# Optimization experiments

Measured on AMD Instinct MI355X. Metric: run time of the kernel, lower is better.

Reference implementation:

```python
import jax, jax.numpy as jnp
import numpy as np

T, B, E, H, F = 1024, 2, 1024, 16, 8
D = E // H
R = 2 * T - 1  # relative positions T-1 .. -(T-1)


def setup_inputs() -> dict:
    key = jax.random.key(0)
    ks = jax.random.split(key, 11)
    std = float(np.sqrt(2.0 / (E + E)))
    return {
        "input": jax.random.normal(ks[0], (T, B, E), jnp.float32),
        "pos": jax.random.normal(ks[1], (R, B, E), jnp.float32),
        "factor": jax.random.normal(ks[2], (F,), jnp.float32),
        "in_proj_weight": jax.random.normal(ks[3], (3 * E * E, F), jnp.float32) * std,
        "pos_proj_weight": jax.random.normal(ks[4], (E * E, F), jnp.float32) * std,
        "out_proj_weight": jax.random.normal(ks[5], (E * E, F), jnp.float32) * std,
        "in_proj_bias": jax.random.normal(ks[6], (3 * E, F), jnp.float32) * 0.02,
        "pos_proj_bias": jax.random.normal(ks[7], (E, F), jnp.float32) * 0.02,
        "out_proj_bias": jax.random.normal(ks[8], (E, F), jnp.float32) * 0.02,
        "r_w_bias": jax.random.normal(ks[9], (E, F), jnp.float32) * 0.02,
        "r_r_bias": jax.random.normal(ks[10], (E, F), jnp.float32) * 0.02,
    }


def _rel_shift(x):
    # x: [BH, T, R] -> out[b, i, j] = x[b, i, j + (T-1) - i]
    bh, q, r = x.shape
    zp = jnp.zeros((bh, q, 1), x.dtype)
    xp = jnp.concatenate([zp, x], axis=2).reshape(bh, r + 1, q)
    return xp[:, 1:, :].reshape(bh, q, r)


def reference(input, pos, factor, in_proj_weight, pos_proj_weight, out_proj_weight,
              in_proj_bias, pos_proj_bias, out_proj_bias, r_w_bias, r_r_bias):
    # hypernetwork: generate effective weights from factor vector (torch.mv)
    W_in = (in_proj_weight @ factor).reshape(3 * E, E)
    W_pos = (pos_proj_weight @ factor).reshape(E, E)
    W_out = (out_proj_weight @ factor).reshape(E, E)
    b_in = in_proj_bias @ factor
    b_pos = pos_proj_bias @ factor
    b_out = out_proj_bias @ factor
    rw = (r_w_bias @ factor).reshape(H, D)  # content bias
    rr = (r_r_bias @ factor).reshape(H, D)  # position bias

    qkv = input @ W_in.T + b_in                      # [T, B, 3E]
    q, k, v = jnp.split(qkv, 3, axis=-1)
    q = q.reshape(T, B, H, D)
    k = k.reshape(T, B, H, D)
    v = v.reshape(T, B, H, D)
    r = (pos @ W_pos.T + b_pos).reshape(R, B, H, D)  # [R, B, H, D]

    scale = 1.0 / np.sqrt(D)
    # AC: content-content + content bias term
    AC = jnp.einsum('ibhd,jbhd->bhij', q + rw, k)    # [B, H, T, T]
    # BD: content-position + position bias term, then relative shift
    BD = jnp.einsum('ibhd,rbhd->bhir', q + rr, r)    # [B, H, T, R]
    BD = _rel_shift(BD.reshape(B * H, T, R))[:, :, :T].reshape(B, H, T, T)

    attn = jax.nn.softmax((AC + BD) * scale, axis=-1)  # [B, H, T, T]
    out = jnp.einsum('bhij,jbhd->ibhd', attn, v).reshape(T, B, E)
    out = out @ W_out.T + b_out                       # [T, B, E]
    return out
```

## Files before the change

kernel.cpp:

```cpp
#include <hip/hip_runtime.h>


typedef _Float16 h16;
typedef _Float16 h16x8 __attribute__((ext_vector_type(8)));
typedef _Float16 h16x4 __attribute__((ext_vector_type(4)));
typedef float f32x4 __attribute__((ext_vector_type(4)));

static __device__ __forceinline__ f32x4 mfma16(h16x8 a, h16x8 b, f32x4 c) {
  return __builtin_amdgcn_mfma_f32_16x16x32_f16(a, b, c, 0, 0, 0);
}
static __device__ __forceinline__ void gload16(const void* g, void* l) {
  __builtin_amdgcn_global_load_lds((const __attribute__((address_space(1))) void*)g,
                                   (__attribute__((address_space(3))) void*)l, 16, 0, 0);
}

__global__ __launch_bounds__(256) void hypernet_kernel(
    const float* __restrict__ fac,
    const float* __restrict__ w_in, const float* __restrict__ w_pos,
    const float* __restrict__ w_out, const float* __restrict__ b_in_w,
    const float* __restrict__ b_pos_w, const float* __restrict__ b_out_w,
    const float* __restrict__ rw_w, const float* __restrict__ rr_w,
    h16* __restrict__ Wall,
    float* __restrict__ bin, float* __restrict__ bpos, float* __restrict__ bout,
    float* __restrict__ rw, float* __restrict__ rr, h16* __restrict__ rb,
    const float* __restrict__ input, const float* __restrict__ pos,
    h16* __restrict__ cast_h)
{
  const int tid = threadIdx.x;
  const float f0=fac[0],f1=fac[1],f2=fac[2],f3=fac[3],
              f4=fac[4],f5=fac[5],f6=fac[6],f7=fac[7];
#define DOT(a,b) ((a).x*f0+(a).y*f1+(a).z*f2+(a).w*f3+(b).x*f4+(b).y*f5+(b).z*f6+(b).w*f7)

  if (blockIdx.x < 2560) {
    const int base = blockIdx.x * 2048 + tid;
    float4 va[8], vb[8];
#pragma unroll
    for (int k = 0; k < 8; ++k) {
      int r = base + k*256;
      const float4* s;
      if (r < 3145728)      s = reinterpret_cast<const float4*>(w_in  + (size_t)r*8);
      else if (r < 4194304) s = reinterpret_cast<const float4*>(w_pos + (size_t)(r-3145728)*8);
      else                  s = reinterpret_cast<const float4*>(w_out + (size_t)(r-4194304)*8);
      va[k] = s[0]; vb[k] = s[1];
    }
#pragma unroll
    for (int k = 0; k < 8; ++k)
      Wall[base + k*256] = (h16)DOT(va[k], vb[k]);
    return;
  }
  if (blockIdx.x < 2596) {
    int idx = (blockIdx.x - 2560) * 256 + tid;
    if (idx < 3072) {
      const float4* s = reinterpret_cast<const float4*>(b_in_w + (size_t)idx*8);
      bin[idx] = DOT(s[0], s[1]); return;
    }
    idx -= 3072;
    if (idx < 1024) {
      const float4* s = reinterpret_cast<const float4*>(b_pos_w + (size_t)idx*8);
      bpos[idx] = DOT(s[0], s[1]); return;
    }
    idx -= 1024;
    if (idx < 1024) {
      const float4* s = reinterpret_cast<const float4*>(b_out_w + (size_t)idx*8);
      bout[idx] = DOT(s[0], s[1]); return;
    }
    idx -= 1024;
    if (idx < 1024) {
      const float4* s = reinterpret_cast<const float4*>(rw_w + (size_t)idx*8);
      rw[idx] = DOT(s[0], s[1]); return;
    }
    idx -= 1024;
    if (idx < 1024) {
      const float4* s = reinterpret_cast<const float4*>(rr_w + (size_t)idx*8);
      rr[idx] = DOT(s[0], s[1]); return;
    }
    idx -= 1024;
    if (idx < 2048)
      rb[(((size_t)(idx >> 6)) << 17) + 2047*64 + (idx & 63)] = (h16)0.f;
    return;
  }
  {
    const int base = (blockIdx.x - 2596) * 2048 + tid;
    float4 v[8]; int g[8];
#pragma unroll
    for (int k = 0; k < 8; ++k) {
      g[k] = base + k*256;
      if (g[k] < 1572352)
        v[k] = (g[k] < 524288) ? reinterpret_cast<const float4*>(input)[g[k]]
                               : reinterpret_cast<const float4*>(pos)[g[k] - 524288];
    }
#pragma unroll
    for (int k = 0; k < 8; ++k)
      if (g[k] < 1572352) {
        h16x4 o = { (h16)v[k].x, (h16)v[k].y, (h16)v[k].z, (h16)v[k].w };
        reinterpret_cast<h16x4*>(cast_h)[g[k]] = o;
      }
  }
#undef DOT
}

template <int MODE>
__global__ __launch_bounds__(256) void gemm_lds_kernel(
    const h16* __restrict__ A, const h16* __restrict__ Bw,
    const float* __restrict__ bias, int M, int N, int K,
    float* __restrict__ Cout,
    const float* __restrict__ rwv, const float* __restrict__ rrv,
    h16* __restrict__ o0, h16* __restrict__ o1,
    h16* __restrict__ o2, h16* __restrict__ o3)
{
  __shared__ __align__(16) h16 a_sm[128*64];
  __shared__ __align__(16) h16 b_sm[128*64];
  const int tid = threadIdx.x, lane = tid & 63, wave = tid >> 6;
  const int quad = lane >> 4, t16 = lane & 15;
  const int wm = wave >> 1, wn = wave & 1;
  const int m0 = blockIdx.y * 128, n0 = blockIdx.x * 128;
  const int lrow = lane >> 3, lgran = lane & 7;
  const int gsw = (lgran ^ lrow) * 8;
  const int xg0 = (quad ^ (t16 & 7)) * 8;
  const int xg1 = xg0 ^ 32;

  f32x4 acc[4][4];
#pragma unroll
  for (int i = 0; i < 4; ++i)
#pragma unroll
    for (int j = 0; j < 4; ++j) acc[i][j] = (f32x4){0.f,0.f,0.f,0.f};

  for (int k0 = 0; k0 < K; k0 += 64) {
    __syncthreads();
#pragma unroll
    for (int s = 0; s < 4; ++s) {
      int rbase = wave*32 + s*8;
      gload16(A  + (size_t)(m0 + rbase + lrow)*K + k0 + gsw, a_sm + rbase*64);
      gload16(Bw + (size_t)(n0 + rbase + lrow)*K + k0 + gsw, b_sm + rbase*64);
    }
    __syncthreads();
#pragma unroll
    for (int kc = 0; kc < 2; ++kc) {
      const int xg = kc ? xg1 : xg0;
      h16x8 af[4], bfr[4];
#pragma unroll
      for (int i = 0; i < 4; ++i) {
        af[i]  = *reinterpret_cast<const h16x8*>(a_sm + (wm*64 + i*16 + t16)*64 + xg);
        bfr[i] = *reinterpret_cast<const h16x8*>(b_sm + (wn*64 + i*16 + t16)*64 + xg);
      }
#pragma unroll
      for (int i = 0; i < 4; ++i)
#pragma unroll
        for (int j = 0; j < 4; ++j)
          acc[i][j] = mfma16(af[i], bfr[j], acc[i][j]);
    }
  }

#pragma unroll
  for (int i = 0; i < 4; ++i) {
    int mb = m0 + wm*64 + i*16 + quad*4;
#pragma unroll
    for (int j = 0; j < 4; ++j) {
      int n = n0 + wn*64 + j*16 + t16;
      float bv = bias[n];
      if (MODE == 2) {
#pragma unroll
        for (int r = 0; r < 4; ++r)
          Cout[(size_t)(mb + r)*N + n] = acc[i][j][r] + bv;
      } else if (MODE == 0) {
        int nn = n & 1023, sec = n >> 10, hh = nn >> 6, d = nn & 63;
        float rwb = rwv[nn], rrb = rrv[nn];
#pragma unroll
        for (int r = 0; r < 4; ++r) {
          int m = mb + r, t = m >> 1, b = m & 1;
          size_t hbase = (size_t)((b << 4) + hh) << 16;
          float v = acc[i][j][r] + bv;
          if (sec == 0)      { o0[hbase + (t << 6) + d] = (h16)(v + rwb);
                               o1[hbase + (t << 6) + d] = (h16)(v + rrb); }
          else if (sec == 1) { o2[hbase + (t << 6) + d] = (h16)v; }
          else               { o3[hbase + (d << 10) + t] = (h16)v; }
        }
      } else {
        int hh = n >> 6, d = n & 63;
#pragma unroll
        for (int r = 0; r < 4; ++r) {
          int m = mb + r;
          if (m < M) {
            int rel = m >> 1, b = m & 1;
            o0[(((size_t)((b << 4) + hh)) << 17) + (rel << 6) + d] = (h16)(acc[i][j][r] + bv);
          }
        }
      }
    }
  }
}

__global__ __launch_bounds__(256) void flash_kernel(
    const h16* __restrict__ qrw, const h16* __restrict__ qrr,
    const h16* __restrict__ kb, const h16* __restrict__ vbt,
    const h16* __restrict__ rb,
    float* __restrict__ o_part, float* __restrict__ ml_part)
{
  __shared__ __align__(16) h16 k_sm[64*64];
  __shared__ __align__(16) h16 vt_sm[64*64];
  __shared__ __align__(16) h16 r_sm[128*64];

  const int tid = threadIdx.x, lane = tid & 63, wave = tid >> 6;
  const int quad = lane >> 4, t16 = lane & 15;
  const int bh = blockIdx.y, i0 = blockIdx.x * 64, jh = blockIdx.z;
  const size_t base  = (size_t)bh << 16;
  const size_t rbase = (size_t)bh << 17;
  const int iw = i0 + wave * 16;
  const int lrow = lane >> 3, lgran = lane & 7;
  const int gsw = (lgran ^ lrow) * 8;
  const int xg0 = (quad ^ (t16 & 7)) * 8;
  const int xg1 = xg0 ^ 32;

  h16x8 a_rw[2], a_rr[2];
  {
    const h16* p = qrw + base + (size_t)(iw + t16)*64 + quad*8;
    a_rw[0] = *reinterpret_cast<const h16x8*>(p);
    a_rw[1] = *reinterpret_cast<const h16x8*>(p + 32);
    const h16* p2 = qrr + base + (size_t)(iw + t16)*64 + quad*8;
    a_rr[0] = *reinterpret_cast<const h16x8*>(p2);
    a_rr[1] = *reinterpret_cast<const h16x8*>(p2 + 32);
  }

  f32x4 o_acc[4];
#pragma unroll
  for (int dc = 0; dc < 4; ++dc) o_acc[dc] = (f32x4){0.f,0.f,0.f,0.f};
  float m_run[4] = {-1e30f,-1e30f,-1e30f,-1e30f};
  float l_run[4] = {0.f,0.f,0.f,0.f};

  h16* bdw = r_sm + wave * (16*84);
  const int cb0 = 3 - wave;

  for (int j0 = jh*256; j0 < jh*256 + 256; j0 += 64) {
    __syncthreads();
    {
#pragma unroll
      for (int s = 0; s < 2; ++s) {
        int row = wave*16 + s*8;
        gload16(kb  + base + (size_t)(j0 + row + lrow)*64 + gsw, k_sm  + row*64);
        gload16(vbt + base + (size_t)(row + lrow)*1024 + j0 + gsw, vt_sm + row*64);
      }
      const int rel0 = j0 - i0 + 960;
#pragma unroll
      for (int s = 0; s < 4; ++s) {
        int row = wave*32 + s*8;
        gload16(rb + rbase + (size_t)(rel0 + row + lrow)*64 + gsw, r_sm + row*64);
      }
    }
    __syncthreads();

    f32x4 s_ac[4];
#pragma unroll
    for (int c = 0; c < 4; ++c) {
      s_ac[c] = (f32x4){0.f,0.f,0.f,0.f};
      s_ac[c] = mfma16(a_rw[0], *reinterpret_cast<const h16x8*>(k_sm + (c*16 + t16)*64 + xg0), s_ac[c]);
      s_ac[c] = mfma16(a_rw[1], *reinterpret_cast<const h16x8*>(k_sm + (c*16 + t16)*64 + xg1), s_ac[c]);
    }
    f32x4 s_bd[5];
#pragma unroll
    for (int u = 0; u < 5; ++u) {
      s_bd[u] = (f32x4){0.f,0.f,0.f,0.f};
      s_bd[u] = mfma16(a_rr[0], *reinterpret_cast<const h16x8*>(r_sm + ((cb0+u)*16 + t16)*64 + xg0), s_bd[u]);
      s_bd[u] = mfma16(a_rr[1], *reinterpret_cast<const h16x8*>(r_sm + ((cb0+u)*16 + t16)*64 + xg1), s_bd[u]);
    }
    __syncthreads();

#pragma unroll
    for (int u = 0; u < 5; ++u)
#pragma unroll
      for (int r = 0; r < 4; ++r)
        bdw[(quad*4 + r)*84 + u*16 + t16] = (h16)s_bd[u][r];

    float sv[4][4];
#pragma unroll
    for (int c = 0; c < 4; ++c)
#pragma unroll
      for (int r = 0; r < 4; ++r) {
        int il = quad*4 + r;
        float bdv = (float)bdw[il*84 + c*16 + t16 + 15 - il];
        sv[c][r] = (s_ac[c][r] + bdv) * 0.125f;
      }

    float alpha[4];
#pragma unroll
    for (int r = 0; r < 4; ++r) {
      float v = fmaxf(fmaxf(sv[0][r], sv[1][r]), fmaxf(sv[2][r], sv[3][r]));
#pragma unroll
      for (int off = 1; off < 16; off <<= 1) v = fmaxf(v, __shfl_xor(v, off, 64));
      float mn = fmaxf(m_run[r], v);
      alpha[r] = __expf(m_run[r] - mn);
      m_run[r] = mn;
    }
#pragma unroll
    for (int r = 0; r < 4; ++r) {
      float s0 = 0.f;
#pragma unroll
      for (int c = 0; c < 4; ++c) {
        float p = __expf(sv[c][r] - m_run[r]);
        sv[c][r] = p; s0 += p;
      }
      l_run[r] = l_run[r]*alpha[r] + s0;
    }
#pragma unroll
    for (int dc = 0; dc < 4; ++dc) {
      f32x4 t = o_acc[dc];
#pragma unroll
      for (int r = 0; r < 4; ++r) t[r] *= alpha[r];
      o_acc[dc] = t;
    }
    h16* pw = bdw;
#pragma unroll
    for (int c = 0; c < 4; ++c)
#pragma unroll
      for (int r = 0; r < 4; ++r)
        pw[(quad*4 + r)*72 + c*16 + t16] = (h16)sv[c][r];

    h16x8 ap0 = *reinterpret_cast<const h16x8*>(pw + t16*72 + quad*8);
    h16x8 ap1 = *reinterpret_cast<const h16x8*>(pw + t16*72 + 32 + quad*8);
#pragma unroll
    for (int dc = 0; dc < 4; ++dc) {
      h16x8 bv0 = *reinterpret_cast<const h16x8*>(vt_sm + (dc*16 + t16)*64 + xg0);
      h16x8 bv1 = *reinterpret_cast<const h16x8*>(vt_sm + (dc*16 + t16)*64 + xg1);
      o_acc[dc] = mfma16(ap0, bv0, o_acc[dc]);
      o_acc[dc] = mfma16(ap1, bv1, o_acc[dc]);
    }
  }

#pragma unroll
  for (int r = 0; r < 4; ++r) {
    float l = l_run[r];
#pragma unroll
    for (int off = 1; off < 16; off <<= 1) l += __shfl_xor(l, off, 64);
    l_run[r] = l;
  }
  const size_t obase = ((size_t)jh*32 + bh) * 1024 * 64;
#pragma unroll
  for (int r = 0; r < 4; ++r) {
    int i = iw + quad*4 + r;
#pragma unroll
    for (int dc = 0; dc < 4; ++dc)
      o_part[obase + (size_t)i*64 + dc*16 + t16] = o_acc[dc][r];
    if (t16 == 0) {
      size_t mo = (((size_t)jh*32 + bh)*1024 + i)*2;
      ml_part[mo]     = m_run[r];
      ml_part[mo + 1] = l_run[r];
    }
  }
}

__global__ __launch_bounds__(256) void combine_kernel(
    const float* __restrict__ o_part, const float* __restrict__ ml_part,
    h16* __restrict__ attn_h)
{
  int gid = blockIdx.x * 256 + threadIdx.x;
  int row = gid >> 4;
  int d4 = (gid & 15) * 4;
  float m[4], l[4];
#pragma unroll
  for (int p = 0; p < 4; ++p) {
    m[p] = ml_part[p*65536 + row*2];
    l[p] = ml_part[p*65536 + row*2 + 1];
  }
  float M = fmaxf(fmaxf(m[0], m[1]), fmaxf(m[2], m[3]));
  float e[4], den = 0.f;
#pragma unroll
  for (int p = 0; p < 4; ++p) { e[p] = __expf(m[p] - M); den += e[p]*l[p]; }
  float inv = 1.f / den;
  float4 acc = {0.f,0.f,0.f,0.f};
#pragma unroll
  for (int p = 0; p < 4; ++p) {
    float4 O = *reinterpret_cast<const float4*>(o_part + (size_t)p*2097152 + (size_t)row*64 + d4);
    acc.x += e[p]*O.x; acc.y += e[p]*O.y; acc.z += e[p]*O.z; acc.w += e[p]*O.w;
  }
  int bh = row >> 10, i = row & 1023, b = bh >> 4, h = bh & 15;
  h16x4 o = { (h16)(acc.x*inv), (h16)(acc.y*inv), (h16)(acc.z*inv), (h16)(acc.w*inv) };
  *reinterpret_cast<h16x4*>(attn_h + ((size_t)(i*2 + b))*1024 + h*64 + d4) = o;
}

extern "C" void kernel_launch(void* const* d_in, const int* in_sizes, int n_in,
                              void* d_out, int out_size, void* d_ws, size_t ws_size,
                              hipStream_t stream)
{
  const float* input  = (const float*)d_in[0];
  const float* pos    = (const float*)d_in[1];
  const float* fac    = (const float*)d_in[2];
  const float* w_in   = (const float*)d_in[3];
  const float* w_pos  = (const float*)d_in[4];
  const float* w_out  = (const float*)d_in[5];
  const float* bin_w  = (const float*)d_in[6];
  const float* bpos_w = (const float*)d_in[7];
  const float* bout_w = (const float*)d_in[8];
  const float* rw_w   = (const float*)d_in[9];
  const float* rr_w   = (const float*)d_in[10];
  float* out = (float*)d_out;
  (void)in_sizes; (void)n_in; (void)out_size; (void)ws_size;

  char* w = (char*)d_ws;
  auto take = [&](size_t bytes) { char* p = w; w += bytes; return p; };
  h16*   Win    = (h16*)take(3145728ull*2);
  h16*   Wpos   = (h16*)take(1048576ull*2);
  h16*   Wout   = (h16*)take(1048576ull*2);
  float* bin    = (float*)take(3072*4);
  float* bpos   = (float*)take(1024*4);
  float* bout   = (float*)take(1024*4);
  float* rw     = (float*)take(1024*4);
  float* rr     = (float*)take(1024*4);
  h16*   in_h   = (h16*)take(2097152ull*2);
  h16*   pos_h  = (h16*)take(4192256ull*2);
  h16*   qrwb   = (h16*)take(2097152ull*2);
  h16*   qrrb   = (h16*)take(2097152ull*2);
  h16*   kb     = (h16*)take(2097152ull*2);
  h16*   vbt    = (h16*)take(2097152ull*2);
  h16*   rb     = (h16*)take(4194304ull*2);
  float* o_part = (float*)take(4ull*2097152ull*4);
  float* ml     = (float*)take(4ull*65536ull*4);
  h16*   attn_h = (h16*)take(2097152ull*2);

  hypernet_kernel<<<3364, 256, 0, stream>>>(fac, w_in, w_pos, w_out, bin_w, bpos_w, bout_w,
                                            rw_w, rr_w, Win, bin, bpos, bout,
                                            rw, rr, rb, input, pos, in_h);
  gemm_lds_kernel<0><<<dim3(24, 16), 256, 0, stream>>>(in_h, Win, bin, 2048, 3072, 1024,
                                                       nullptr, rw, rr, qrwb, qrrb, kb, vbt);
  gemm_lds_kernel<1><<<dim3(8, 32), 256, 0, stream>>>(pos_h, Wpos, bpos, 4094, 1024, 1024,
                                                      nullptr, nullptr, nullptr, rb, nullptr, nullptr, nullptr);
  flash_kernel<<<dim3(16, 32, 4), 256, 0, stream>>>(qrwb, qrrb, kb, vbt, rb, o_part, ml);
  combine_kernel<<<2048, 256, 0, stream>>>(o_part, ml, attn_h);
  gemm_lds_kernel<2><<<dim3(8, 16), 256, 0, stream>>>(attn_h, Wout, bout, 2048, 1024, 1024,
                                                      out, nullptr, nullptr, nullptr, nullptr, nullptr, nullptr);
}
```

Before: 371.1 us.

## Restructure hypernet weight generation and move V transpose to a separate kernel

The hypernet weight pass now gives each block a contiguous 4096-row slab and software-pipelines its loads with a prefetch of the next chunk. The input cast uses one float4 per thread across many more blocks. The QKV GEMM epilogue now writes V in [t,d] order, where it previously did a strided transposed store, and a new small LDS-tiled kernel produces the transposed V for the flash kernel. This aims to remove uncoalesced scattered stores in the GEMM epilogue and improve streaming bandwidth in the hypernet pass, at the cost of an extra launch and an extra round trip of V through memory.

New measurement: 364.2 us. About the same (-1.9%).

```diff
diff --git a/kernel.cpp b/kernel.cpp
--- a/kernel.cpp
+++ b/kernel.cpp
@@ -14,7 +14,7 @@
                                    (__attribute__((address_space(3))) void*)l, 16, 0, 0);
 }
 
-__global__ __launch_bounds__(256) void hypernet_kernel(
+__global__ __launch_bounds__(256, 2) void hypernet_kernel(
     const float* __restrict__ fac,
     const float* __restrict__ w_in, const float* __restrict__ w_pos,
     const float* __restrict__ w_out, const float* __restrict__ b_in_w,
@@ -31,25 +31,35 @@
               f4=fac[4],f5=fac[5],f6=fac[6],f7=fac[7];
 #define DOT(a,b) ((a).x*f0+(a).y*f1+(a).z*f2+(a).w*f3+(b).x*f4+(b).y*f5+(b).z*f6+(b).w*f7)
 
-  if (blockIdx.x < 2560) {
-    const int base = blockIdx.x * 2048 + tid;
-    float4 va[8], vb[8];
-#pragma unroll
-    for (int k = 0; k < 8; ++k) {
-      int r = base + k*256;
-      const float4* s;
-      if (r < 3145728)      s = reinterpret_cast<const float4*>(w_in  + (size_t)r*8);
-      else if (r < 4194304) s = reinterpret_cast<const float4*>(w_pos + (size_t)(r-3145728)*8);
-      else                  s = reinterpret_cast<const float4*>(w_out + (size_t)(r-4194304)*8);
-      va[k] = s[0]; vb[k] = s[1];
-    }
-#pragma unroll
-    for (int k = 0; k < 8; ++k)
-      Wall[base + k*256] = (h16)DOT(va[k], vb[k]);
+  if (blockIdx.x < 1280) {
+    const int b = blockIdx.x;
+    const float* tbl; size_t rowbase;
+    if (b < 768)       { tbl = w_in;  rowbase = (size_t)b*4096; }
+    else if (b < 1024) { tbl = w_pos; rowbase = (size_t)b*4096 - 3145728; }
+    else               { tbl = w_out; rowbase = (size_t)b*4096 - 4194304; }
+    const size_t outbase = (size_t)b*4096;
+    float4 cur[4], nxt[4];
+    {
+      const float4* p0 = reinterpret_cast<const float4*>(tbl + (rowbase + tid)*8);
+      const float4* p1 = reinterpret_cast<const float4*>(tbl + (rowbase + 256 + tid)*8);
+      cur[0]=p0[0]; cur[1]=p0[1]; cur[2]=p1[0]; cur[3]=p1[1];
+    }
+#pragma unroll
+    for (int s = 0; s < 8; ++s) {
+      if (s < 7) {
+        const float4* p0 = reinterpret_cast<const float4*>(tbl + (rowbase + (s+1)*512 + tid)*8);
+        const float4* p1 = reinterpret_cast<const float4*>(tbl + (rowbase + (s+1)*512 + 256 + tid)*8);
+        nxt[0]=p0[0]; nxt[1]=p0[1]; nxt[2]=p1[0]; nxt[3]=p1[1];
+      }
+      Wall[outbase + s*512 + tid]       = (h16)DOT(cur[0], cur[1]);
+      Wall[outbase + s*512 + 256 + tid] = (h16)DOT(cur[2], cur[3]);
+#pragma unroll
+      for (int q = 0; q < 4; ++q) cur[q] = nxt[q];
+    }
     return;
   }
-  if (blockIdx.x < 2596) {
-    int idx = (blockIdx.x - 2560) * 256 + tid;
+  if (blockIdx.x < 1316) {
+    int idx = (blockIdx.x - 1280) * 256 + tid;
     if (idx < 3072) {
       const float4* s = reinterpret_cast<const float4*>(b_in_w + (size_t)idx*8);
       bin[idx] = DOT(s[0], s[1]); return;
@@ -80,21 +90,11 @@
     return;
   }
   {
-    const int base = (blockIdx.x - 2596) * 2048 + tid;
-    float4 v[8]; int g[8];
-#pragma unroll
-    for (int k = 0; k < 8; ++k) {
-      g[k] = base + k*256;
-      if (g[k] < 1572352)
-        v[k] = (g[k] < 524288) ? reinterpret_cast<const float4*>(input)[g[k]]
-                               : reinterpret_cast<const float4*>(pos)[g[k] - 524288];
-    }
-#pragma unroll
-    for (int k = 0; k < 8; ++k)
-      if (g[k] < 1572352) {
-        h16x4 o = { (h16)v[k].x, (h16)v[k].y, (h16)v[k].z, (h16)v[k].w };
-        reinterpret_cast<h16x4*>(cast_h)[g[k]] = o;
-      }
+    const int g = (blockIdx.x - 1316) * 256 + tid;
+    float4 v = (g < 524288) ? reinterpret_cast<const float4*>(input)[g]
+                            : reinterpret_cast<const float4*>(pos)[g - 524288];
+    h16x4 o = { (h16)v.x, (h16)v.y, (h16)v.z, (h16)v.w };
+    reinterpret_cast<h16x4*>(cast_h)[g] = o;
   }
 #undef DOT
 }
@@ -168,12 +168,11 @@
 #pragma unroll
         for (int r = 0; r < 4; ++r) {
           int m = mb + r, t = m >> 1, b = m & 1;
-          size_t hbase = (size_t)((b << 4) + hh) << 16;
+          size_t off = ((size_t)((b << 4) + hh) << 16) + (t << 6) + d;
           float v = acc[i][j][r] + bv;
-          if (sec == 0)      { o0[hbase + (t << 6) + d] = (h16)(v + rwb);
-                               o1[hbase + (t << 6) + d] = (h16)(v + rrb); }
-          else if (sec == 1) { o2[hbase + (t << 6) + d] = (h16)v; }
-          else               { o3[hbase + (d << 10) + t] = (h16)v; }
+          if (sec == 0)      { o0[off] = (h16)(v + rwb); o1[off] = (h16)(v + rrb); }
+          else if (sec == 1) { o2[off] = (h16)v; }
+          else               { o3[off] = (h16)v; }
         }
       } else {
         int hh = n >> 6, d = n & 63;
@@ -188,6 +187,27 @@
       }
     }
   }
+}
+
+__global__ __launch_bounds__(256) void transpose_v_kernel(
+    const h16* __restrict__ vb, h16* __restrict__ vbt)
+{
+  __shared__ h16 tile[64*72];
+  const int bh = blockIdx.y, t0 = blockIdx.x * 64;
+  const int r = threadIdx.x >> 3, c = (threadIdx.x & 7) * 8;
+  const h16* src = vb + ((size_t)bh << 16) + (size_t)(t0 + r)*64 + c;
+  *reinterpret_cast<h16x8*>(tile + r*72 + c)        = *reinterpret_cast<const h16x8*>(src);
+  *reinterpret_cast<h16x8*>(tile + (r + 32)*72 + c) = *reinterpret_cast<const h16x8*>(src + 32*64);
+  __syncthreads();
+  h16x8 o0, o1;
+#pragma unroll
+  for (int e = 0; e < 8; ++e) {
+    o0[e] = tile[(c + e)*72 + r];
+    o1[e] = tile[(c + e)*72 + r + 32];
+  }
+  h16* dst = vbt + ((size_t)bh << 16) + (size_t)r*1024 + t0 + c;
+  *reinterpret_cast<h16x8*>(dst)            = o0;
+  *reinterpret_cast<h16x8*>(dst + 32*1024)  = o1;
 }
 
 __global__ __launch_bounds__(256) void flash_kernel(
@@ -409,19 +429,21 @@
   h16*   qrwb   = (h16*)take(2097152ull*2);
   h16*   qrrb   = (h16*)take(2097152ull*2);
   h16*   kb     = (h16*)take(2097152ull*2);
+  h16*   vb     = (h16*)take(2097152ull*2);
   h16*   vbt    = (h16*)take(2097152ull*2);
   h16*   rb     = (h16*)take(4194304ull*2);
   float* o_part = (float*)take(4ull*2097152ull*4);
   float* ml     = (float*)take(4ull*65536ull*4);
   h16*   attn_h = (h16*)take(2097152ull*2);
 
-  hypernet_kernel<<<3364, 256, 0, stream>>>(fac, w_in, w_pos, w_out, bin_w, bpos_w, bout_w,
+  hypernet_kernel<<<7458, 256, 0, stream>>>(fac, w_in, w_pos, w_out, bin_w, bpos_w, bout_w,
                                             rw_w, rr_w, Win, bin, bpos, bout,
                                             rw, rr, rb, input, pos, in_h);
   gemm_lds_kernel<0><<<dim3(24, 16), 256, 0, stream>>>(in_h, Win, bin, 2048, 3072, 1024,
-                                                       nullptr, rw, rr, qrwb, qrrb, kb, vbt);
+                                                       nullptr, rw, rr, qrwb, qrrb, kb, vb);
   gemm_lds_kernel<1><<<dim3(8, 32), 256, 0, stream>>>(pos_h, Wpos, bpos, 4094, 1024, 1024,
                                                       nullptr, nullptr, nullptr, rb, nullptr, nullptr, nullptr);
+  transpose_v_kernel<<<dim3(16, 32), 256, 0, stream>>>(vb, vbt);
   flash_kernel<<<dim3(16, 32, 4), 256, 0, stream>>>(qrwb, qrrb, kb, vbt, rb, o_part, ml);
   combine_kernel<<<2048, 256, 0, stream>>>(o_part, ml, attn_h);
   gemm_lds_kernel<2><<<dim3(8, 16), 256, 0, stream>>>(attn_h, Wout, bout, 2048, 1024, 1024,
```
